# Performance work log

Measured on AMD Instinct MI355X. Metric: run time of the kernel, lower is better.

Reference implementation:

```python
import jax, jax.numpy as jnp
import numpy as np

HIDDEN = 128; HEADS = 8; HD = HIDDEN // HEADS; NRBF = 50; NLAYERS = 6
CUT = 5.0; MAXZ = 100
N = 5000; E = 100000


def cosine_cutoff(d):
    # cutoff_lower = 0: 0.5*(cos(pi*d/cut)+1) * (d < cut)
    return 0.5 * (jnp.cos(d * (jnp.pi / CUT)) + 1.0) * (d < CUT)


def expnorm_rbf(d, means, betas):
    # ExpNormalSmearing with cutoff_lower=0, alpha = 5/cutoff
    alpha = 5.0 / CUT
    return cosine_cutoff(d)[:, None] * jnp.exp(-betas * (jnp.exp(-alpha * d)[:, None] - means) ** 2)


def layernorm(x, w, b):
    m = x.mean(-1, keepdims=True)
    v = ((x - m) ** 2).mean(-1, keepdims=True)
    return (x - m) / jnp.sqrt(v + 1e-5) * w + b


def setup_inputs():
    key = jax.random.key(0)
    ks = jax.random.split(key, 16)
    start = float(np.exp(-CUT))

    def lin(k, fi, fo):
        return jax.random.normal(k, (fi, fo), jnp.float32) / np.sqrt(fi)

    def lin_l(k, fi, fo):
        return jax.random.normal(k, (NLAYERS, fi, fo), jnp.float32) / np.sqrt(fi)

    return {
        "z": jax.random.randint(ks[0], (N,), 0, MAXZ),
        "edge_index": jax.random.randint(ks[1], (2, E), 0, N),
        "edge_vec": jax.random.normal(ks[2], (E, 3), jnp.float32) * 1.7,
        "emb": jax.random.normal(ks[3], (MAXZ, HIDDEN), jnp.float32),
        "means": jnp.linspace(start, 1.0, NRBF, dtype=jnp.float32),
        "betas": jnp.full((NRBF,), (2.0 / NRBF * (1.0 - start)) ** -2, dtype=jnp.float32),
        "ne_emb": jax.random.normal(ks[4], (MAXZ, HIDDEN), jnp.float32),
        "dpW": lin(ks[5], NRBF, HIDDEN), "dpb": jnp.zeros((HIDDEN,), jnp.float32),
        "cbW": lin(ks[6], 2 * HIDDEN, HIDDEN), "cbb": jnp.zeros((HIDDEN,), jnp.float32),
        "lnw": jnp.ones((NLAYERS, HIDDEN), jnp.float32), "lnb": jnp.zeros((NLAYERS, HIDDEN), jnp.float32),
        "qW": lin_l(ks[7], HIDDEN, HIDDEN), "qb": jnp.zeros((NLAYERS, HIDDEN), jnp.float32),
        "kW": lin_l(ks[8], HIDDEN, HIDDEN), "kb": jnp.zeros((NLAYERS, HIDDEN), jnp.float32),
        "vW": lin_l(ks[9], HIDDEN, 3 * HIDDEN), "vb": jnp.zeros((NLAYERS, 3 * HIDDEN), jnp.float32),
        "oW": lin_l(ks[10], HIDDEN, 3 * HIDDEN), "ob": jnp.zeros((NLAYERS, 3 * HIDDEN), jnp.float32),
        "vecW": lin_l(ks[11], HIDDEN, 3 * HIDDEN),
        "dkW": lin_l(ks[12], NRBF, HIDDEN), "dkb": jnp.zeros((NLAYERS, HIDDEN), jnp.float32),
        "dvW": lin_l(ks[13], NRBF, 3 * HIDDEN), "dvb": jnp.zeros((NLAYERS, 3 * HIDDEN), jnp.float32),
        "onw": jnp.ones((HIDDEN,), jnp.float32), "onb": jnp.zeros((HIDDEN,), jnp.float32),
    }


def _forward(z, edge_index, edge_vec, emb, means, betas, ne_emb, dpW, dpb, cbW, cbb,
             lnw, lnb, qW, qb, kW, kb, vW, vb, oW, ob, vecW, dkW, dkb, dvW, dvb, onw, onb):
    src, dst = edge_index[0], edge_index[1]          # j (source), i (target)
    n = z.shape[0]
    x = emb[z]                                        # [N, H]
    ew = jnp.linalg.norm(edge_vec, axis=1)            # [E]
    ea = expnorm_rbf(ew, means, betas)                # [E, NRBF]
    nonself = src != dst
    # normalize edge vectors except self-loop edges (kept as-is, matching the torch clone/mask)
    evn = edge_vec / jnp.where(nonself, ew, 1.0)[:, None]
    cut_e = cosine_cutoff(ew)                         # [E]

    # --- NeighborEmbedding: self-loops removed from aggregation ---
    W = (ea @ dpW + dpb) * cut_e[:, None]
    W = jnp.where(nonself[:, None], W, 0.0)
    agg = jax.ops.segment_sum(ne_emb[z][src] * W, dst, num_segments=n)
    x = jnp.concatenate([x, agg], axis=1) @ cbW + cbb
    vec = jnp.zeros((n, 3, HIDDEN), x.dtype)

    def layer(carry, p):
        x, vec = carry
        h = layernorm(x, p["lnw"], p["lnb"])
        q = (h @ p["qW"] + p["qb"]).reshape(n, HEADS, HD)
        k = (h @ p["kW"] + p["kb"]).reshape(n, HEADS, HD)
        v = (h @ p["vW"] + p["vb"]).reshape(n, HEADS, 3 * HD)
        vec1, vec2, vec3 = jnp.split(jnp.einsum("nch,hk->nck", vec, p["vecW"]), 3, axis=-1)
        vec_dot = (vec1 * vec2).sum(axis=1)                    # [N, H]
        vec_h = vec.reshape(n, 3, HEADS, HD)
        dk = jax.nn.silu(ea @ p["dkW"] + p["dkb"]).reshape(-1, HEADS, HD)
        dv = jax.nn.silu(ea @ p["dvW"] + p["dvb"]).reshape(-1, HEADS, 3 * HD)
        # per-edge attention weight, silu activation, smoothly cut off
        attn = jax.nn.silu((q[dst] * k[src] * dk).sum(-1)) * cut_e[:, None]   # [E, heads]
        xm, w1, w2 = jnp.split(v[src] * dv, 3, axis=2)                        # each [E, heads, HD]
        xm = xm * attn[:, :, None]
        vecm = vec_h[src] * w1[:, None] + w2[:, None] * evn[:, :, None, None] # [E, 3, heads, HD]
        xa = jax.ops.segment_sum(xm, dst, num_segments=n).reshape(n, HIDDEN)
        va = jax.ops.segment_sum(vecm, dst, num_segments=n).reshape(n, 3, HIDDEN)
        o1, o2, o3 = jnp.split(xa @ p["oW"] + p["ob"], 3, axis=-1)
        dx = vec_dot * o2 + o3
        dvec = vec3 * o1[:, None, :] + va
        return (x + dx, vec + dvec), None

    stacked = {"lnw": lnw, "lnb": lnb, "qW": qW, "qb": qb, "kW": kW, "kb": kb,
               "vW": vW, "vb": vb, "oW": oW, "ob": ob, "vecW": vecW,
               "dkW": dkW, "dkb": dkb, "dvW": dvW, "dvb": dvb}
    (x, vec), _ = jax.lax.scan(layer, (x, vec), stacked)
    x = layernorm(x, onw, onb)
    return x, vec


def reference(z, edge_index, edge_vec, emb, means, betas, ne_emb, dpW, dpb, cbW, cbb,
              lnw, lnb, qW, qb, kW, kb, vW, vb, oW, ob, vecW, dkW, dkb, dvW, dvb, onw, onb):
    return _forward(z, edge_index, edge_vec, emb, means, betas, ne_emb, dpW, dpb, cbW, cbb,
                    lnw, lnb, qW, qb, kW, kb, vW, vb, oW, ob, vecW, dkW, dkb, dvW, dvb, onw, onb)
```

## Files before the change

kernel.cpp:

```cpp
#include <hip/hip_runtime.h>
#include <math.h>

#define HID 128
#define NRBF 50
#define NLAYERS 6
#define CUTV 5.0f
#define KNOTS 1024
#define TSCALE 204.8f
#define TINV   0.0048828125f
#define TROWS  (KNOTS + 1)
#define TRWORDS 512
#define TSTRIDE ((size_t)TROWS * TRWORDS)
#define WCOLS 1408
#define KB 16

typedef unsigned int  uint32;
typedef unsigned short ushort16;
typedef __attribute__((ext_vector_type(8))) short short8;
typedef __attribute__((ext_vector_type(4))) float f32x4;

__device__ __forceinline__ float siluf(float x){ return x / (1.0f + __expf(-x)); }
__device__ __forceinline__ float lerpf(float a, float b, float f){ return fmaf(f, b - a, a); }
__device__ __forceinline__ ushort16 f2b(float x){
    uint32 u = __float_as_uint(x);
    u += 0x7fffu + ((u >> 16) & 1u);
    return (ushort16)(u >> 16);
}
__device__ __forceinline__ float b2f(ushort16 u){ return __uint_as_float(((uint32)u) << 16); }
__device__ __forceinline__ uint32 packp(float a, float b){
    return (uint32)f2b(a) | ((uint32)f2b(b) << 16);
}
__device__ __forceinline__ float plo(uint32 u){ return __uint_as_float(u << 16); }
__device__ __forceinline__ float phi(uint32 u){ return __uint_as_float(u & 0xffff0000u); }
__device__ __forceinline__ float plerp(uint32 u, float f){ float a = plo(u); return fmaf(f, phi(u) - a, a); }

__global__ void k_zero(int* p, int n){
    int i = blockIdx.x*blockDim.x + threadIdx.x;
    if (i < n) p[i] = 0;
}

__global__ void k_count(const int* ei, int E, int* counts){
    int e = blockIdx.x*blockDim.x + threadIdx.x;
    if (e < E) atomicAdd(&counts[ei[E + e]], 1);
}

__global__ void k_scan(const int* counts, int* offsets, int* cursor, int n){
    __shared__ int part[1024];
    int tid = threadIdx.x;
    int PER = (n + 1023) >> 10;
    int base = tid * PER;
    int loc[8]; int s = 0;
    #pragma unroll 8
    for (int ii = 0; ii < 8; ii++){
        if (ii < PER){
            int idx = base + ii;
            int c = (idx < n) ? counts[idx] : 0;
            loc[ii] = s; s += c;
        }
    }
    part[tid] = s;
    __syncthreads();
    for (int off = 1; off < 1024; off <<= 1){
        int v = (tid >= off) ? part[tid - off] : 0;
        __syncthreads();
        part[tid] += v;
        __syncthreads();
    }
    int excl = (tid == 0) ? 0 : part[tid - 1];
    #pragma unroll 8
    for (int ii = 0; ii < 8; ii++){
        if (ii < PER){
            int idx = base + ii;
            if (idx < n){ int o = excl + loc[ii]; offsets[idx] = o; cursor[idx] = o; }
        }
    }
    if (tid == 1023) offsets[n] = part[1023];
}

__global__ void k_scatter(const int* ei, int E, int* cursor, int* eperm){
    int e = blockIdx.x*blockDim.x + threadIdx.x;
    if (e < E){
        int d = ei[E + e];
        int pos = atomicAdd(&cursor[d], 1);
        eperm[pos] = e;
    }
}

__global__ __launch_bounds__(256) void k_srcsort(const int* offsets, const int* ei, int* eperm, int N){
    int node = blockIdx.x*4 + (threadIdx.x >> 6);
    int lane = threadIdx.x & 63;
    if (node >= N) return;
    int r0 = offsets[node], r1 = offsets[node+1];
    for (int c0 = r0; c0 < r1; c0 += 64){
        int n = min(64, r1 - c0);
        int e = 0; int key = 0x7fffffff;
        if (lane < n){ e = eperm[c0 + lane]; key = ei[e]; }
        int rank = 0;
        for (int t = 0; t < n; t++){
            int kt = __shfl(key, t, 64);
            if (t != lane && ((kt < key) || (kt == key && t < lane))) rank++;
        }
        if (lane < n) eperm[c0 + rank] = e;
    }
}

__global__ void k_edge_vals(const int* ei, const float* edge_vec, const int* eperm, int E,
                            int4* edata, float4* evn4){
    int row = blockIdx.x*blockDim.x + threadIdx.x;
    if (row >= E) return;
    int e = eperm[row];
    int s = ei[e], d = ei[E + e];
    float vx = edge_vec[e*3+0], vy = edge_vec[e*3+1], vz = edge_vec[e*3+2];
    float ew = sqrtf(vx*vx + vy*vy + vz*vz);
    float cut = (ew < CUTV) ? 0.5f*(__cosf(ew * 0.62831853071795864f) + 1.0f) : 0.0f;
    int ns = (s != d) ? 1 : 0;
    float inv = ns ? (1.0f/ew) : 1.0f;
    float un = fminf(ew * TSCALE, (float)KNOTS);
    int j = (int)un;
    float f = un - (float)j;
    int4 ed; ed.x = s; ed.y = j; ed.z = __float_as_int(f); ed.w = __float_as_int(cut);
    edata[row] = ed;
    float4 ev; ev.x = vx*inv; ev.y = vy*inv; ev.z = vz*inv; ev.w = ns ? 1.0f : 0.0f;
    evn4[row] = ev;
}

__global__ void k_pad(ushort16* hb16, ushort16* vecm, ushort16* xab16, int N, int Nup, int N3up){
    int i = blockIdx.x*blockDim.x + threadIdx.x;
    int hpad = (Nup - N)*HID;
    int vpad = (N3up - 3*N)*HID;
    if (i < hpad){ hb16[(size_t)N*HID + i] = 0; xab16[(size_t)N*HID + i] = 0; }
    if (i < vpad) vecm[(size_t)3*N*HID + i] = 0;
}

__global__ __launch_bounds__(512) void k_build_tables(
    const float* means, const float* betas,
    const float* dkW, const float* dkb, const float* dvW, const float* dvb,
    uint32* Tp){
    int jb = blockIdx.x * KB;
    int l  = blockIdx.y;
    int c  = threadIdx.x;
    __shared__ float ea_s[KB+1][NRBF+2];
    for (int idx = c; idx < (KB+1)*NRBF; idx += 512){
        int kk = idx / NRBF, r = idx - kk*NRBF;
        float d = (jb + kk) * TINV;
        float cut = (d < CUTV) ? 0.5f*(__cosf(d * 0.62831853071795864f) + 1.0f) : 0.0f;
        float u = __expf(-d) - means[r];
        ea_s[kk][r] = cut * __expf(-betas[r]*u*u);
    }
    __syncthreads();
    int h = c >> 2, i = c & 3;
    const float* Wcol; int stride; float bias;
    if (i == 0){
        Wcol = dkW + (size_t)l*NRBF*HID + h; stride = HID;
        bias = dkb[(size_t)l*HID + h];
    } else {
        int col = ((h >> 4)*48 + (h & 15)) + 16*(i-1);
        Wcol = dvW + (size_t)l*NRBF*384 + col; stride = 384;
        bias = dvb[(size_t)l*384 + col];
    }
    float a[KB+1];
    #pragma unroll
    for (int k = 0; k <= KB; k++) a[k] = bias;
    for (int r = 0; r < NRBF; r++){
        float w = Wcol[(size_t)r*stride];
        #pragma unroll
        for (int k = 0; k <= KB; k++) a[k] += ea_s[k][r]*w;
    }
    uint32* dst = Tp + (size_t)l*TSTRIDE + (size_t)jb*TRWORDS + c;
    float sp = siluf(a[0]);
    #pragma unroll
    for (int k = 0; k < KB; k++){
        int j = jb + k;
        if (j >= TROWS) break;
        float sn = siluf(a[k+1]);
        dst[(size_t)k*TRWORDS] = packp(sp, sn);
        sp = sn;
    }
}

__global__ __launch_bounds__(128) void k_build_ne(
    const float* means, const float* betas,
    const float* dpW, const float* dpb, float2* Tne){
    int j = blockIdx.x, c = threadIdx.x;
    __shared__ float ea0[NRBF], ea1[NRBF];
    float d0 = j * TINV, d1 = (j+1) * TINV;
    float c0 = (d0 < CUTV) ? 0.5f*(__cosf(d0 * 0.62831853071795864f) + 1.0f) : 0.0f;
    float c1 = (d1 < CUTV) ? 0.5f*(__cosf(d1 * 0.62831853071795864f) + 1.0f) : 0.0f;
    if (c < NRBF){
        float m = means[c], be = betas[c];
        float u0 = __expf(-d0) - m, u1 = __expf(-d1) - m;
        ea0[c] = c0 * __expf(-be*u0*u0);
        ea1[c] = c1 * __expf(-be*u1*u1);
    }
    __syncthreads();
    float a0 = dpb[c], a1 = a0;
    #pragma unroll
    for (int r = 0; r < NRBF; r++){ float w = dpW[r*HID + c]; a0 += ea0[r]*w; a1 += ea1[r]*w; }
    float2 o; o.x = a0*c0; o.y = a1*c1;
    Tne[(size_t)j*HID + c] = o;
}

__global__ __launch_bounds__(256) void k_build_wt(
    const float* qW, const float* kW, const float* vW, const float* vecW, const float* oW,
    ushort16* WT){
    int l = blockIdx.y; int c0 = blockIdx.x*32;
    __shared__ ushort16 t[128][33];
    for (int i = threadIdx.x; i < 128*32; i += 256){
        int k = i >> 5, c = i & 31;
        int gcol = c0 + c;
        const float* W; int C; int oc;
        if (gcol < 128)      { W = qW   + (size_t)l*HID*128; C = 128; oc = gcol; }
        else if (gcol < 640) {
            int s = gcol - 128; int h = s >> 2, si = s & 3;
            if (si == 3){ W = kW + (size_t)l*HID*128; C = 128; oc = h; }
            else        { W = vW + (size_t)l*HID*384; C = 384; oc = (h>>4)*48 + (h&15) + 16*si; }
        }
        else if (gcol < 1024){ W = vecW + (size_t)l*HID*384; C = 384; oc = gcol-640; }
        else                 { W = oW   + (size_t)l*HID*384; C = 384; oc = gcol-1024; }
        t[k][c] = f2b(W[(size_t)k*C + oc]);
    }
    __syncthreads();
    ushort16* dst = WT + (size_t)l*WCOLS*HID + (size_t)c0*HID;
    for (int i = threadIdx.x; i < 128*32; i += 256){
        int c = i >> 7, k = i & 127;
        dst[(size_t)c*HID + k] = t[k][c];
    }
}

__global__ __launch_bounds__(512) void k_build_bias(
    const float* kb, const float* vb, float* kvbias){
    int l = blockIdx.x, s = threadIdx.x;
    int h = s >> 2, i = s & 3;
    float v = (i == 3) ? kb[(size_t)l*HID + h]
                       : vb[(size_t)l*384 + (h>>4)*48 + (h&15) + 16*i];
    kvbias[(size_t)l*512 + s] = v;
}

__global__ __launch_bounds__(256) void k_mfma01(
    const ushort16* __restrict__ hb16, const ushort16* __restrict__ vecm,
    const ushort16* __restrict__ WT, const float* __restrict__ qbias,
    const float* __restrict__ kvbias,
    float* __restrict__ qo, ushort16* __restrict__ vpack,
    ushort16* __restrict__ vecout, int N){
    int cg = blockIdx.x;
    int rblk = blockIdx.y*64;
    const ushort16* A; int R; int cblk; const ushort16* wt;
    if (cg < 10){ A = hb16; R = N;   cblk = cg*64;      wt = WT; }
    else        { A = vecm; R = 3*N; cblk = (cg-10)*64; wt = WT + (size_t)640*HID; }
    if (rblk >= R) return;
    int wave = threadIdx.x >> 6, lane = threadIdx.x & 63;
    int r0 = rblk + wave*16;
    int l16 = lane & 15, lg = lane >> 4;
    short8 a[4];
    const ushort16* ar = A + (size_t)(r0 + l16)*HID + lg*8;
    #pragma unroll
    for (int ks = 0; ks < 4; ks++) a[ks] = *(const short8*)(ar + ks*32);
    f32x4 acc[4];
    #pragma unroll
    for (int ct = 0; ct < 4; ct++){ acc[ct][0]=0.f; acc[ct][1]=0.f; acc[ct][2]=0.f; acc[ct][3]=0.f; }
    #pragma unroll
    for (int ct = 0; ct < 4; ct++){
        const ushort16* br = wt + (size_t)(cblk + ct*16 + l16)*HID + lg*8;
        #pragma unroll
        for (int ks = 0; ks < 4; ks++){
            short8 b = *(const short8*)(br + ks*32);
            acc[ct] = __builtin_amdgcn_mfma_f32_16x16x32_bf16(a[ks], b, acc[ct], 0, 0, 0);
        }
    }
    __shared__ ushort16 lds[64][72];
    if (cg < 2){
        #pragma unroll
        for (int ct = 0; ct < 4; ct++){
            int gc = cblk + ct*16 + l16;
            float bb = qbias[gc];
            #pragma unroll
            for (int rg = 0; rg < 4; rg++){
                int row = r0 + lg*4 + rg;
                if (row < R) qo[(size_t)row*HID + gc] = acc[ct][rg] + bb;
            }
        }
        return;
    }
    const float* bias = (cg < 10) ? (kvbias + (cblk - 128)) : nullptr;
    #pragma unroll
    for (int ct = 0; ct < 4; ct++){
        int lc = ct*16 + l16;
        float bb = bias ? bias[lc] : 0.f;
        #pragma unroll
        for (int rg = 0; rg < 4; rg++)
            lds[wave*16 + lg*4 + rg][lc] = f2b(acc[ct][rg] + bb);
    }
    __syncthreads();
    ushort16* out; int stride, colbase;
    if (cg < 10){ out = vpack;  stride = 512; colbase = cblk - 128; }
    else        { out = vecout; stride = 384; colbase = cblk; }
    const uint32* l32 = (const uint32*)&lds[0][0];
    #pragma unroll
    for (int it = 0; it < 8; it++){
        int idx = it*256 + threadIdx.x;
        int row = idx >> 5, cp = idx & 31;
        int grow = rblk + row;
        if (grow < R){
            uint32 val = l32[row*36 + cp];
            *((uint32*)(out + (size_t)grow*stride + colbase) + cp) = val;
        }
    }
}

__global__ __launch_bounds__(128) void k_ne_agg(
    const int* offsets, const int4* edata, const float4* evn4, const float2* Tne,
    const int* z, const float* ne_emb, float* agg){
    int i = blockIdx.x, h = threadIdx.x;
    float acc = 0.f;
    int r0 = offsets[i], r1 = offsets[i+1];
    #pragma unroll 4
    for (int row = r0; row < r1; row++){
        int4 ed = edata[row];
        int s = ed.x, j = ed.y;
        float f = __int_as_float(ed.z);
        float mask = evn4[row].w;
        float2 tv = Tne[(size_t)j*HID + h];
        float w = lerpf(tv.x, tv.y, f) * mask;
        acc += w * ne_emb[(size_t)z[s]*HID + h];
    }
    agg[(size_t)i*HID + h] = acc;
}

__global__ __launch_bounds__(128) void k_combine_ln(
    const int* z, const float* emb, const float* agg, const float* cbW, const float* cbb,
    const float* lnw0, const float* lnb0,
    float* x, ushort16* hb16, float* vec, ushort16* vecm, uint32* vecpack, int N){
    int n0 = blockIdx.x*8, h = threadIdx.x;
    __shared__ float in_s[8][2*HID];
    int nr = min(8, N - n0);
    for (int m = 0; m < nr; m++){
        in_s[m][h]       = emb[(size_t)z[n0+m]*HID + h];
        in_s[m][HID + h] = agg[(size_t)(n0+m)*HID + h];
    }
    __syncthreads();
    float acc[8];
    #pragma unroll
    for (int m = 0; m < 8; m++) acc[m] = 0.f;
    for (int kk = 0; kk < 2*HID; kk += 4){
        float w0 = cbW[(kk+0)*HID + h], w1 = cbW[(kk+1)*HID + h];
        float w2 = cbW[(kk+2)*HID + h], w3 = cbW[(kk+3)*HID + h];
        #pragma unroll
        for (int m = 0; m < 8; m++){
            const float* a = &in_s[m][kk];
            acc[m] += a[0]*w0 + a[1]*w1 + a[2]*w2 + a[3]*w3;
        }
    }
    float bias = cbb[h], w = lnw0[h], bb = lnb0[h];
    __shared__ float r1_[2], r2_[2];
    int wid = h >> 6;
    for (int m = 0; m < nr; m++){
        int n = n0 + m;
        float v = acc[m] + bias;
        x[(size_t)n*HID + h] = v;
        float s1 = v, s2 = v*v;
        #pragma unroll
        for (int o = 32; o; o >>= 1){ s1 += __shfl_xor(s1, o, 64); s2 += __shfl_xor(s2, o, 64); }
        if ((h & 63) == 0){ r1_[wid] = s1; r2_[wid] = s2; }
        __syncthreads();
        float sum = r1_[0] + r1_[1], sumsq = r2_[0] + r2_[1];
        float mean = sum * (1.f/HID);
        float var = sumsq * (1.f/HID) - mean*mean;
        float inv = rsqrtf(var + 1e-5f);
        hb16[(size_t)n*HID + h] = f2b((v - mean)*inv*w + bb);
        __syncthreads();
        vec [(size_t)n*384 + h]       = 0.f;
        vec [(size_t)n*384 + 128 + h] = 0.f;
        vec [(size_t)n*384 + 256 + h] = 0.f;
        vecm[(size_t)n*384 + h]       = 0;
        vecm[(size_t)n*384 + 128 + h] = 0;
        vecm[(size_t)n*384 + 256 + h] = 0;
        vecpack[(size_t)n*256 + 2*h]     = 0;
        vecpack[(size_t)n*256 + 2*h + 1] = 0;
    }
}

__global__ __launch_bounds__(128) void k_edge_agg(
    const int* __restrict__ offsets, const int4* __restrict__ edata,
    const float4* __restrict__ evn4, const uint32* __restrict__ Tp,
    const float* __restrict__ q, const ushort16* __restrict__ vpack,
    const uint32* __restrict__ vecpack,
    ushort16* __restrict__ xa16, float* __restrict__ va){
    int i = blockIdx.x, h = threadIdx.x;
    float qv = q[(size_t)i*HID + h];
    float axa = 0.f, av0 = 0.f, av1 = 0.f, av2 = 0.f;
    int r0 = offsets[i], r1 = offsets[i+1];
    for (int t0 = r0; t0 < r1; t0 += 4){
        float f_[4], cut_[4], ex_[4], ey_[4], ez_[4];
        uint4 t4_[4];
        uint2 vp_[4], vc_[4];
        #pragma unroll
        for (int u = 0; u < 4; u++){
            int row = min(t0 + u, r1 - 1);
            int4 ed = edata[row];
            int s = ed.x, j = ed.y;
            f_[u]   = __int_as_float(ed.z);
            cut_[u] = __int_as_float(ed.w);
            t4_[u] = *(const uint4*)(Tp + (size_t)j*TRWORDS + 4*h);
            vp_[u] = *(const uint2*)(vpack + (size_t)s*512 + 4*h);
            vc_[u] = *(const uint2*)(vecpack + (size_t)s*256 + 2*h);
            float4 ev = evn4[row];
            ex_[u] = ev.x; ey_[u] = ev.y; ez_[u] = ev.z;
        }
        #pragma unroll
        for (int u = 0; u < 4; u++){
            if (t0 + u >= r1) break;
            float f = f_[u];
            float dk = plerp(t4_[u].x, f);
            float kv = phi(vp_[u].y);
            float p = qv * kv * dk;
            p += __shfl_xor(p, 1, 64);
            p += __shfl_xor(p, 2, 64);
            p += __shfl_xor(p, 4, 64);
            p += __shfl_xor(p, 8, 64);
            float attn = siluf(p) * cut_[u];
            float dv0 = plerp(t4_[u].y, f);
            float dv1 = plerp(t4_[u].z, f);
            float dv2 = plerp(t4_[u].w, f);
            axa += plo(vp_[u].x) * dv0 * attn;
            float w1v = phi(vp_[u].x) * dv1;
            float w2v = plo(vp_[u].y) * dv2;
            av0 += plo(vc_[u].x)*w1v + w2v*ex_[u];
            av1 += phi(vc_[u].x)*w1v + w2v*ey_[u];
            av2 += plo(vc_[u].y)*w1v + w2v*ez_[u];
        }
    }
    xa16[(size_t)i*HID + h] = f2b(axa);
    va[(size_t)i*384 + h]       = av0;
    va[(size_t)i*384 + 128 + h] = av1;
    va[(size_t)i*384 + 256 + h] = av2;
}

#define OROWS 32
__global__ __launch_bounds__(256) void k_oupd(
    const ushort16* __restrict__ xab16, const ushort16* __restrict__ WT,
    const float* __restrict__ obias,
    float* __restrict__ x, float* __restrict__ vec, ushort16* __restrict__ vecm,
    uint32* __restrict__ vecpack,
    const ushort16* __restrict__ vecout, const float* __restrict__ va,
    const float* __restrict__ lnw_n, const float* __restrict__ lnb_n,
    ushort16* __restrict__ hb16, float* __restrict__ outx, float* __restrict__ outv,
    int N, int fin){
    __shared__ float o_s[OROWS][385];
    int tile = blockIdx.x; int r0 = tile*OROWS;
    int wid = threadIdx.x >> 6, lane = threadIdx.x & 63;
    int l16 = lane & 15, lg = lane >> 4;
    {
        int rr = r0 + (wid & 1)*16;
        const ushort16* ar = xab16 + (size_t)(rr + l16)*HID + lg*8;
        short8 a[4];
        #pragma unroll
        for (int ks = 0; ks < 4; ks++) a[ks] = *(const short8*)(ar + ks*32);
        int cbase = (wid >> 1)*192;
        const ushort16* wt = WT + (size_t)1024*HID;
        #pragma unroll
        for (int ct = 0; ct < 12; ct++){
            f32x4 acc; acc[0]=0.f; acc[1]=0.f; acc[2]=0.f; acc[3]=0.f;
            const ushort16* br = wt + (size_t)(cbase + ct*16 + l16)*HID + lg*8;
            #pragma unroll
            for (int ks = 0; ks < 4; ks++){
                short8 b = *(const short8*)(br + ks*32);
                acc = __builtin_amdgcn_mfma_f32_16x16x32_bf16(a[ks], b, acc, 0, 0, 0);
            }
            int gc = cbase + ct*16 + l16;
            float bb = obias[gc];
            #pragma unroll
            for (int rg = 0; rg < 4; rg++)
                o_s[(wid & 1)*16 + lg*4 + rg][gc] = acc[rg] + bb;
        }
    }
    __syncthreads();
    for (int pass = 0; pass < 8; pass++){
        int nrow = pass*4 + wid;
        int n = r0 + nrow;
        if (n >= N) break;
        const ushort16* vo = vecout + (size_t)n*1152;
        const float* o_r = o_s[nrow];
        size_t vb = (size_t)n*384;
        float xva, xvb, v0a, v0b, v1a, v1b, v2a, v2b;
        #pragma unroll
        for (int half = 0; half < 2; half++){
            int hh = lane + half*64;
            float vdot = b2f(vo[hh])*b2f(vo[128+hh]) + b2f(vo[384+hh])*b2f(vo[512+hh])
                       + b2f(vo[768+hh])*b2f(vo[896+hh]);
            float o1 = o_r[hh], o2 = o_r[128+hh], o3 = o_r[256+hh];
            float xv = x[(size_t)n*HID + hh] + vdot*o2 + o3;
            float v0 = vec[vb + hh]       + b2f(vo[256  + hh])*o1 + va[vb + hh];
            float v1 = vec[vb + 128 + hh] + b2f(vo[640  + hh])*o1 + va[vb + 128 + hh];
            float v2 = vec[vb + 256 + hh] + b2f(vo[1024 + hh])*o1 + va[vb + 256 + hh];
            if (half == 0){ xva = xv; v0a = v0; v1a = v1; v2a = v2; }
            else          { xvb = xv; v0b = v0; v1b = v1; v2b = v2; }
        }
        float s1 = xva + xvb, s2 = xva*xva + xvb*xvb;
        #pragma unroll
        for (int o = 32; o; o >>= 1){ s1 += __shfl_xor(s1, o, 64); s2 += __shfl_xor(s2, o, 64); }
        float mean = s1 * (1.f/HID);
        float var = s2 * (1.f/HID) - mean*mean;
        float inv = rsqrtf(var + 1e-5f);
        #pragma unroll
        for (int half = 0; half < 2; half++){
            int hh = lane + half*64;
            float xv = half ? xvb : xva;
            float v0 = half ? v0b : v0a;
            float v1 = half ? v1b : v1a;
            float v2 = half ? v2b : v2a;
            float lnv = (xv - mean)*inv*lnw_n[hh] + lnb_n[hh];
            if (!fin){
                x[(size_t)n*HID + hh] = xv;
                vec[vb + hh] = v0; vec[vb + 128 + hh] = v1; vec[vb + 256 + hh] = v2;
                vecm[vb + hh] = f2b(v0); vecm[vb + 128 + hh] = f2b(v1); vecm[vb + 256 + hh] = f2b(v2);
                vecpack[(size_t)n*256 + 2*hh]     = packp(v0, v1);
                vecpack[(size_t)n*256 + 2*hh + 1] = packp(v2, 0.f);
                hb16[(size_t)n*HID + hh] = f2b(lnv);
            } else {
                outx[(size_t)n*HID + hh] = lnv;
                outv[vb + hh] = v0; outv[vb + 128 + hh] = v1; outv[vb + 256 + hh] = v2;
            }
        }
    }
}

extern "C" void kernel_launch(void* const* d_in, const int* in_sizes, int n_in,
                              void* d_out, int out_size, void* d_ws, size_t ws_size,
                              hipStream_t stream){
    const int*   z        = (const int*)  d_in[0];
    const int*   ei       = (const int*)  d_in[1];
    const float* edge_vec = (const float*)d_in[2];
    const float* emb      = (const float*)d_in[3];
    const float* means    = (const float*)d_in[4];
    const float* betas    = (const float*)d_in[5];
    const float* ne_emb   = (const float*)d_in[6];
    const float* dpW      = (const float*)d_in[7];
    const float* dpb      = (const float*)d_in[8];
    const float* cbW      = (const float*)d_in[9];
    const float* cbb      = (const float*)d_in[10];
    const float* lnw      = (const float*)d_in[11];
    const float* lnb      = (const float*)d_in[12];
    const float* qW       = (const float*)d_in[13];
    const float* qb       = (const float*)d_in[14];
    const float* kW       = (const float*)d_in[15];
    const float* kb       = (const float*)d_in[16];
    const float* vW       = (const float*)d_in[17];
    const float* vb       = (const float*)d_in[18];
    const float* oW       = (const float*)d_in[19];
    const float* obias    = (const float*)d_in[20];
    const float* vecW     = (const float*)d_in[21];
    const float* dkW      = (const float*)d_in[22];
    const float* dkb      = (const float*)d_in[23];
    const float* dvW      = (const float*)d_in[24];
    const float* dvb      = (const float*)d_in[25];
    const float* onw      = (const float*)d_in[26];
    const float* onb      = (const float*)d_in[27];

    int N = in_sizes[0];
    int E = in_sizes[1] / 2;
    int Nup  = ((N + 63) >> 6) << 6;
    int N3up = ((3*N + 63) >> 6) << 6;

    char* p = (char*)d_ws;
    auto alloc = [&](size_t bytes){ void* r = (void*)p; p += (bytes + 255) & ~(size_t)255; return r; };
    int*      counts  = (int*)     alloc((size_t)N*4);
    int*      offsets = (int*)     alloc((size_t)(N+1)*4);
    int*      cursor  = (int*)     alloc((size_t)N*4);
    int*      eperm   = (int*)     alloc((size_t)E*4);
    int4*     edata   = (int4*)    alloc((size_t)E*16);
    float4*   evn4    = (float4*)  alloc((size_t)E*16);
    uint32*   Tp      = (uint32*)  alloc((size_t)NLAYERS*TSTRIDE*4);
    float2*   Tne     = (float2*)  alloc((size_t)TROWS*HID*8);
    ushort16* WT      = (ushort16*)alloc((size_t)NLAYERS*WCOLS*HID*2);
    float*    kvbias  = (float*)   alloc((size_t)NLAYERS*512*4);
    float*    agg     = (float*)   alloc((size_t)N*HID*4);
    float*    xb      = (float*)   alloc((size_t)N*HID*4);
    ushort16* hb16    = (ushort16*)alloc((size_t)Nup*HID*2);
    float*    qb_     = (float*)   alloc((size_t)N*HID*4);
    ushort16* vpack   = (ushort16*)alloc((size_t)N*512*2);
    uint32*   vecpack = (uint32*)  alloc((size_t)N*256*4);
    ushort16* vecm    = (ushort16*)alloc((size_t)N3up*HID*2);
    float*    vecb    = (float*)   alloc((size_t)N*384*4);
    ushort16* vecout  = (ushort16*)alloc((size_t)N*1152*2);
    ushort16* xab16   = (ushort16*)alloc((size_t)Nup*HID*2);
    float*    vab     = (float*)   alloc((size_t)N*384*4);

    k_zero<<<(N+255)/256, 256, 0, stream>>>(counts, N);
    k_count<<<(E+255)/256, 256, 0, stream>>>(ei, E, counts);
    k_scan<<<1, 1024, 0, stream>>>(counts, offsets, cursor, N);
    k_scatter<<<(E+255)/256, 256, 0, stream>>>(ei, E, cursor, eperm);
    k_srcsort<<<(N+3)/4, 256, 0, stream>>>(offsets, ei, eperm, N);
    k_edge_vals<<<(E+255)/256, 256, 0, stream>>>(ei, edge_vec, eperm, E, edata, evn4);
    k_pad<<<((Nup-N)*HID + (N3up-3*N)*HID + 255)/256 + 1, 256, 0, stream>>>(hb16, vecm, xab16, N, Nup, N3up);

    k_build_tables<<<dim3((TROWS + KB - 1)/KB, NLAYERS), 512, 0, stream>>>(means, betas, dkW, dkb, dvW, dvb, Tp);
    k_build_ne<<<TROWS, 128, 0, stream>>>(means, betas, dpW, dpb, Tne);
    k_build_wt<<<dim3(WCOLS/32, NLAYERS), 256, 0, stream>>>(qW, kW, vW, vecW, oW, WT);
    k_build_bias<<<NLAYERS, 512, 0, stream>>>(kb, vb, kvbias);
    k_ne_agg<<<N, 128, 0, stream>>>(offsets, edata, evn4, Tne, z, ne_emb, agg);
    k_combine_ln<<<(N+7)/8, 128, 0, stream>>>(z, emb, agg, cbW, cbb, lnw, lnb,
                                              xb, hb16, vecb, vecm, vecpack, N);

    float* outx = (float*)d_out;
    float* outv = (float*)d_out + (size_t)N*HID;

    for (int l = 0; l < NLAYERS; l++){
        const ushort16* WTl = WT + (size_t)l*WCOLS*HID;
        k_mfma01<<<dim3(16, (3*N+63)/64), 256, 0, stream>>>(hb16, vecm, WTl,
            qb + (size_t)l*HID, kvbias + (size_t)l*512,
            qb_, vpack, vecout, N);
        k_edge_agg<<<N, 128, 0, stream>>>(offsets, edata, evn4, Tp + (size_t)l*TSTRIDE,
                                          qb_, vpack, vecpack, xab16, vab);
        int fin = (l == NLAYERS-1);
        k_oupd<<<(N + OROWS - 1)/OROWS, 256, 0, stream>>>(xab16, WTl, obias + (size_t)l*384,
            xb, vecb, vecm, vecpack, vecout, vab,
            fin ? onw : lnw + (size_t)(l+1)*HID,
            fin ? onb : lnb + (size_t)(l+1)*HID,
            hb16, outx, outv, N, fin);
    }
}
```

Baseline: 670.4 us.

## Remap edge-agg to one wavefront per node with two channels per lane

Each node's edge aggregation now runs on a single 64-lane wavefront, packed four nodes per 256-thread block, and each lane handles channels g and g+64. The per-layer tables, q, vpack and vecpack are re-laid out so each lane's two channels sit next to each other, which allows wider 128-bit loads. This halves the number of edge-metadata loads and loop iterations per channel and cuts the block count. The producing kernels must write the new interleaved layout consistently, and the extra registers may lower occupancy.

After: 704.7 us. 5.1% more time.

```diff
diff --git a/kernel.cpp b/kernel.cpp
--- a/kernel.cpp
+++ b/kernel.cpp
@@ -166,7 +166,8 @@
         #pragma unroll
         for (int k = 0; k <= KB; k++) a[k] += ea_s[k][r]*w;
     }
-    uint32* dst = Tp + (size_t)l*TSTRIDE + (size_t)jb*TRWORDS + c;
+    int slot = (h & 63)*8 + (h >> 6)*4 + i;
+    uint32* dst = Tp + (size_t)l*TSTRIDE + (size_t)jb*TRWORDS + slot;
     float sp = siluf(a[0]);
     #pragma unroll
     for (int k = 0; k < KB; k++){
@@ -273,10 +274,11 @@
         for (int ct = 0; ct < 4; ct++){
             int gc = cblk + ct*16 + l16;
             float bb = qbias[gc];
+            int qslot = (gc & 63)*2 + (gc >> 6);
             #pragma unroll
             for (int rg = 0; rg < 4; rg++){
                 int row = r0 + lg*4 + rg;
-                if (row < R) qo[(size_t)row*HID + gc] = acc[ct][rg] + bb;
+                if (row < R) qo[(size_t)row*HID + qslot] = acc[ct][rg] + bb;
             }
         }
         return;
@@ -291,18 +293,32 @@
             lds[wave*16 + lg*4 + rg][lc] = f2b(acc[ct][rg] + bb);
     }
     __syncthreads();
-    ushort16* out; int stride, colbase;
-    if (cg < 10){ out = vpack;  stride = 512; colbase = cblk - 128; }
-    else        { out = vecout; stride = 384; colbase = cblk; }
     const uint32* l32 = (const uint32*)&lds[0][0];
-    #pragma unroll
-    for (int it = 0; it < 8; it++){
-        int idx = it*256 + threadIdx.x;
-        int row = idx >> 5, cp = idx & 31;
-        int grow = rblk + row;
-        if (grow < R){
-            uint32 val = l32[row*36 + cp];
-            *((uint32*)(out + (size_t)grow*stride + colbase) + cp) = val;
+    if (cg < 10){
+        int colbase = cblk - 128;
+        #pragma unroll
+        for (int it = 0; it < 8; it++){
+            int idx = it*256 + threadIdx.x;
+            int row = idx >> 5, cp = idx & 31;
+            int grow = rblk + row;
+            if (grow < R){
+                uint32 val = l32[row*36 + cp];
+                int s0 = colbase + 2*cp;
+                int hh = s0 >> 2, w = (s0 & 3) >> 1;
+                int slot = (hh & 63)*4 + (hh >> 6)*2 + w;
+                ((uint32*)(vpack + (size_t)grow*512))[slot] = val;
+            }
+        }
+    } else {
+        #pragma unroll
+        for (int it = 0; it < 8; it++){
+            int idx = it*256 + threadIdx.x;
+            int row = idx >> 5, cp = idx & 31;
+            int grow = rblk + row;
+            if (grow < R){
+                uint32 val = l32[row*36 + cp];
+                *((uint32*)(vecout + (size_t)grow*384 + cblk) + cp) = val;
+            }
         }
     }
 }
@@ -379,20 +395,22 @@
     }
 }
 
-__global__ __launch_bounds__(128) void k_edge_agg(
+__global__ __launch_bounds__(256) void k_edge_agg(
     const int* __restrict__ offsets, const int4* __restrict__ edata,
     const float4* __restrict__ evn4, const uint32* __restrict__ Tp,
     const float* __restrict__ q, const ushort16* __restrict__ vpack,
     const uint32* __restrict__ vecpack,
-    ushort16* __restrict__ xa16, float* __restrict__ va){
-    int i = blockIdx.x, h = threadIdx.x;
-    float qv = q[(size_t)i*HID + h];
-    float axa = 0.f, av0 = 0.f, av1 = 0.f, av2 = 0.f;
-    int r0 = offsets[i], r1 = offsets[i+1];
+    ushort16* __restrict__ xa16, float* __restrict__ va, int N){
+    int node = blockIdx.x*4 + (threadIdx.x >> 6);
+    int g = threadIdx.x & 63;
+    if (node >= N) return;
+    float2 qv = *(const float2*)(q + (size_t)node*HID + 2*g);
+    float axaA = 0.f, av0A = 0.f, av1A = 0.f, av2A = 0.f;
+    float axaB = 0.f, av0B = 0.f, av1B = 0.f, av2B = 0.f;
+    int r0 = offsets[node], r1 = offsets[node+1];
     for (int t0 = r0; t0 < r1; t0 += 4){
         float f_[4], cut_[4], ex_[4], ey_[4], ez_[4];
-        uint4 t4_[4];
-        uint2 vp_[4], vc_[4];
+        uint4 ta_[4], tb_[4], vp_[4], vc_[4];
         #pragma unroll
         for (int u = 0; u < 4; u++){
             int row = min(t0 + u, r1 - 1);
@@ -400,39 +418,49 @@
             int s = ed.x, j = ed.y;
             f_[u]   = __int_as_float(ed.z);
             cut_[u] = __int_as_float(ed.w);
-            t4_[u] = *(const uint4*)(Tp + (size_t)j*TRWORDS + 4*h);
-            vp_[u] = *(const uint2*)(vpack + (size_t)s*512 + 4*h);
-            vc_[u] = *(const uint2*)(vecpack + (size_t)s*256 + 2*h);
+            const uint32* tp = Tp + (size_t)j*TRWORDS + 8*g;
+            ta_[u] = *(const uint4*)(tp);
+            tb_[u] = *(const uint4*)(tp + 4);
+            vp_[u] = *(const uint4*)((const uint32*)(vpack + (size_t)s*512) + 4*g);
+            vc_[u] = *(const uint4*)(vecpack + (size_t)s*256 + 4*g);
             float4 ev = evn4[row];
             ex_[u] = ev.x; ey_[u] = ev.y; ez_[u] = ev.z;
         }
         #pragma unroll
         for (int u = 0; u < 4; u++){
             if (t0 + u >= r1) break;
-            float f = f_[u];
-            float dk = plerp(t4_[u].x, f);
-            float kv = phi(vp_[u].y);
-            float p = qv * kv * dk;
-            p += __shfl_xor(p, 1, 64);
-            p += __shfl_xor(p, 2, 64);
-            p += __shfl_xor(p, 4, 64);
-            p += __shfl_xor(p, 8, 64);
-            float attn = siluf(p) * cut_[u];
-            float dv0 = plerp(t4_[u].y, f);
-            float dv1 = plerp(t4_[u].z, f);
-            float dv2 = plerp(t4_[u].w, f);
-            axa += plo(vp_[u].x) * dv0 * attn;
-            float w1v = phi(vp_[u].x) * dv1;
-            float w2v = plo(vp_[u].y) * dv2;
-            av0 += plo(vc_[u].x)*w1v + w2v*ex_[u];
-            av1 += phi(vc_[u].x)*w1v + w2v*ey_[u];
-            av2 += plo(vc_[u].y)*w1v + w2v*ez_[u];
-        }
-    }
-    xa16[(size_t)i*HID + h] = f2b(axa);
-    va[(size_t)i*384 + h]       = av0;
-    va[(size_t)i*384 + 128 + h] = av1;
-    va[(size_t)i*384 + 256 + h] = av2;
+            float f = f_[u], cut = cut_[u];
+            float kA = phi(vp_[u].y);
+            float pA = qv.x * kA * plerp(ta_[u].x, f);
+            float kB = phi(vp_[u].w);
+            float pB = qv.y * kB * plerp(tb_[u].x, f);
+            pA += __shfl_xor(pA, 1, 64); pB += __shfl_xor(pB, 1, 64);
+            pA += __shfl_xor(pA, 2, 64); pB += __shfl_xor(pB, 2, 64);
+            pA += __shfl_xor(pA, 4, 64); pB += __shfl_xor(pB, 4, 64);
+            pA += __shfl_xor(pA, 8, 64); pB += __shfl_xor(pB, 8, 64);
+            float attnA = siluf(pA) * cut;
+            float attnB = siluf(pB) * cut;
+            axaA += plo(vp_[u].x) * plerp(ta_[u].y, f) * attnA;
+            axaB += plo(vp_[u].z) * plerp(tb_[u].y, f) * attnB;
+            float w1A = phi(vp_[u].x) * plerp(ta_[u].z, f);
+            float w2A = plo(vp_[u].y) * plerp(ta_[u].w, f);
+            float w1B = phi(vp_[u].z) * plerp(tb_[u].z, f);
+            float w2B = plo(vp_[u].w) * plerp(tb_[u].w, f);
+            float ex = ex_[u], ey = ey_[u], ez = ez_[u];
+            av0A += plo(vc_[u].x)*w1A + w2A*ex;
+            av1A += phi(vc_[u].x)*w1A + w2A*ey;
+            av2A += plo(vc_[u].y)*w1A + w2A*ez;
+            av0B += plo(vc_[u].z)*w1B + w2B*ex;
+            av1B += phi(vc_[u].z)*w1B + w2B*ey;
+            av2B += plo(vc_[u].w)*w1B + w2B*ez;
+        }
+    }
+    xa16[(size_t)node*HID + g]      = f2b(axaA);
+    xa16[(size_t)node*HID + g + 64] = f2b(axaB);
+    float* var_ = va + (size_t)node*384;
+    var_[g]            = av0A; var_[g + 64]       = av0B;
+    var_[128 + g]      = av1A; var_[128 + g + 64] = av1B;
+    var_[256 + g]      = av2A; var_[256 + g + 64] = av2B;
 }
 
 #define OROWS 32
@@ -513,8 +541,9 @@
                 x[(size_t)n*HID + hh] = xv;
                 vec[vb + hh] = v0; vec[vb + 128 + hh] = v1; vec[vb + 256 + hh] = v2;
                 vecm[vb + hh] = f2b(v0); vecm[vb + 128 + hh] = f2b(v1); vecm[vb + 256 + hh] = f2b(v2);
-                vecpack[(size_t)n*256 + 2*hh]     = packp(v0, v1);
-                vecpack[(size_t)n*256 + 2*hh + 1] = packp(v2, 0.f);
+                int gg = hh & 63, hf = hh >> 6;
+                vecpack[(size_t)n*256 + gg*4 + hf*2]     = packp(v0, v1);
+                vecpack[(size_t)n*256 + gg*4 + hf*2 + 1] = packp(v2, 0.f);
                 hb16[(size_t)n*HID + hh] = f2b(lnv);
             } else {
                 outx[(size_t)n*HID + hh] = lnv;
@@ -609,8 +638,8 @@
         k_mfma01<<<dim3(16, (3*N+63)/64), 256, 0, stream>>>(hb16, vecm, WTl,
             qb + (size_t)l*HID, kvbias + (size_t)l*512,
             qb_, vpack, vecout, N);
-        k_edge_agg<<<N, 128, 0, stream>>>(offsets, edata, evn4, Tp + (size_t)l*TSTRIDE,
-                                          qb_, vpack, vecpack, xab16, vab);
+        k_edge_agg<<<(N+3)/4, 256, 0, stream>>>(offsets, edata, evn4, Tp + (size_t)l*TSTRIDE,
+                                                qb_, vpack, vecpack, xab16, vab, N);
         int fin = (l == NLAYERS-1);
         k_oupd<<<(N + OROWS - 1)/OROWS, 256, 0, stream>>>(xab16, WTl, obias + (size_t)l*384,
             xb, vecb, vecm, vecpack, vecout, vab,
```

## Compact mfma01 grid, bf16-pack neighbor-embedding tables, batch ne_agg loads

Applied to the files above, without the earlier changes.

The k_mfma01 launch becomes a flat 1D grid with no early-exit blocks, so the many empty blocks the 2D grid spent on the hidden-state columns go away. The neighbor-embedding table and the per-node gathered ne_emb are stored as packed bf16, which halves the gather traffic in k_ne_agg. That loop now issues four edges' loads before accumulating, and masks self-loops by comparing the source index instead of reading evn4. The zero kernel is replaced with hipMemsetAsync; bf16 storage adds some rounding in the initial embedding.

Measured after the change: 615.2 us. 8.2% less time.

```diff
diff --git a/kernel.cpp b/kernel.cpp
--- a/kernel.cpp
+++ b/kernel.cpp
@@ -33,11 +33,6 @@
 __device__ __forceinline__ float plo(uint32 u){ return __uint_as_float(u << 16); }
 __device__ __forceinline__ float phi(uint32 u){ return __uint_as_float(u & 0xffff0000u); }
 __device__ __forceinline__ float plerp(uint32 u, float f){ float a = plo(u); return fmaf(f, phi(u) - a, a); }
-
-__global__ void k_zero(int* p, int n){
-    int i = blockIdx.x*blockDim.x + threadIdx.x;
-    if (i < n) p[i] = 0;
-}
 
 __global__ void k_count(const int* ei, int E, int* counts){
     int e = blockIdx.x*blockDim.x + threadIdx.x;
@@ -132,6 +127,13 @@
     if (i < vpad) vecm[(size_t)3*N*HID + i] = 0;
 }
 
+__global__ void k_prep_nemb(const int* z, const float* ne_emb, ushort16* nemb16, int total){
+    int idx = blockIdx.x*256 + threadIdx.x;
+    if (idx >= total) return;
+    int n = idx >> 7, h = idx & 127;
+    nemb16[idx] = f2b(ne_emb[(size_t)z[n]*HID + h]);
+}
+
 __global__ __launch_bounds__(512) void k_build_tables(
     const float* means, const float* betas,
     const float* dkW, const float* dkb, const float* dvW, const float* dvb,
@@ -180,7 +182,7 @@
 
 __global__ __launch_bounds__(128) void k_build_ne(
     const float* means, const float* betas,
-    const float* dpW, const float* dpb, float2* Tne){
+    const float* dpW, const float* dpb, uint32* Tne32){
     int j = blockIdx.x, c = threadIdx.x;
     __shared__ float ea0[NRBF], ea1[NRBF];
     float d0 = j * TINV, d1 = (j+1) * TINV;
@@ -196,8 +198,7 @@
     float a0 = dpb[c], a1 = a0;
     #pragma unroll
     for (int r = 0; r < NRBF; r++){ float w = dpW[r*HID + c]; a0 += ea0[r]*w; a1 += ea1[r]*w; }
-    float2 o; o.x = a0*c0; o.y = a1*c1;
-    Tne[(size_t)j*HID + c] = o;
+    Tne32[(size_t)j*HID + c] = packp(a0*c0, a1*c1);
 }
 
 __global__ __launch_bounds__(256) void k_build_wt(
@@ -242,12 +243,15 @@
     const float* __restrict__ kvbias,
     float* __restrict__ qo, ushort16* __restrict__ vpack,
     ushort16* __restrict__ vecout, int N){
-    int cg = blockIdx.x;
-    int rblk = blockIdx.y*64;
+    int NT1 = (N + 63) >> 6;
+    int NT3 = (3*N + 63) >> 6;
+    int b = blockIdx.x;
+    int cg, rblk;
+    if (b < 10*NT1){ cg = b / NT1; rblk = (b - cg*NT1)*64; }
+    else { int b2 = b - 10*NT1; int c2 = b2 / NT3; cg = 10 + c2; rblk = (b2 - c2*NT3)*64; }
     const ushort16* A; int R; int cblk; const ushort16* wt;
     if (cg < 10){ A = hb16; R = N;   cblk = cg*64;      wt = WT; }
     else        { A = vecm; R = 3*N; cblk = (cg-10)*64; wt = WT + (size_t)640*HID; }
-    if (rblk >= R) return;
     int wave = threadIdx.x >> 6, lane = threadIdx.x & 63;
     int r0 = rblk + wave*16;
     int l16 = lane & 15, lg = lane >> 4;
@@ -263,8 +267,8 @@
         const ushort16* br = wt + (size_t)(cblk + ct*16 + l16)*HID + lg*8;
         #pragma unroll
         for (int ks = 0; ks < 4; ks++){
-            short8 b = *(const short8*)(br + ks*32);
-            acc[ct] = __builtin_amdgcn_mfma_f32_16x16x32_bf16(a[ks], b, acc[ct], 0, 0, 0);
+            short8 bfr = *(const short8*)(br + ks*32);
+            acc[ct] = __builtin_amdgcn_mfma_f32_16x16x32_bf16(a[ks], bfr, acc[ct], 0, 0, 0);
         }
     }
     __shared__ ushort16 lds[64][72];
@@ -308,20 +312,28 @@
 }
 
 __global__ __launch_bounds__(128) void k_ne_agg(
-    const int* offsets, const int4* edata, const float4* evn4, const float2* Tne,
-    const int* z, const float* ne_emb, float* agg){
+    const int* __restrict__ offsets, const int4* __restrict__ edata,
+    const uint32* __restrict__ Tne32, const ushort16* __restrict__ nemb16,
+    float* __restrict__ agg){
     int i = blockIdx.x, h = threadIdx.x;
     float acc = 0.f;
     int r0 = offsets[i], r1 = offsets[i+1];
-    #pragma unroll 4
-    for (int row = r0; row < r1; row++){
-        int4 ed = edata[row];
-        int s = ed.x, j = ed.y;
-        float f = __int_as_float(ed.z);
-        float mask = evn4[row].w;
-        float2 tv = Tne[(size_t)j*HID + h];
-        float w = lerpf(tv.x, tv.y, f) * mask;
-        acc += w * ne_emb[(size_t)z[s]*HID + h];
+    for (int t0 = r0; t0 < r1; t0 += 4){
+        uint32 tn_[4]; ushort16 nb_[4]; float f_[4]; int s_[4];
+        #pragma unroll
+        for (int u = 0; u < 4; u++){
+            int row = min(t0 + u, r1 - 1);
+            int4 ed = edata[row];
+            s_[u] = ed.x;
+            f_[u] = __int_as_float(ed.z);
+            tn_[u] = Tne32[(size_t)ed.y*HID + h];
+            nb_[u] = nemb16[(size_t)ed.x*HID + h];
+        }
+        #pragma unroll
+        for (int u = 0; u < 4; u++){
+            if (t0 + u >= r1) break;
+            if (s_[u] != i) acc += plerp(tn_[u], f_[u]) * b2f(nb_[u]);
+        }
     }
     agg[(size_t)i*HID + h] = acc;
 }
@@ -401,7 +413,7 @@
             f_[u]   = __int_as_float(ed.z);
             cut_[u] = __int_as_float(ed.w);
             t4_[u] = *(const uint4*)(Tp + (size_t)j*TRWORDS + 4*h);
-            vp_[u] = *(const uint2*)(vpack + (size_t)s*512 + 4*h);
+            vp_[u] = *(const uint2*)((const uint32*)(vpack + (size_t)s*512) + 2*h);
             vc_[u] = *(const uint2*)(vecpack + (size_t)s*256 + 2*h);
             float4 ev = evn4[row];
             ex_[u] = ev.x; ey_[u] = ev.y; ez_[u] = ev.z;
@@ -570,9 +582,10 @@
     int4*     edata   = (int4*)    alloc((size_t)E*16);
     float4*   evn4    = (float4*)  alloc((size_t)E*16);
     uint32*   Tp      = (uint32*)  alloc((size_t)NLAYERS*TSTRIDE*4);
-    float2*   Tne     = (float2*)  alloc((size_t)TROWS*HID*8);
+    uint32*   Tne32   = (uint32*)  alloc((size_t)TROWS*HID*4);
     ushort16* WT      = (ushort16*)alloc((size_t)NLAYERS*WCOLS*HID*2);
     float*    kvbias  = (float*)   alloc((size_t)NLAYERS*512*4);
+    ushort16* nemb16  = (ushort16*)alloc((size_t)N*HID*2);
     float*    agg     = (float*)   alloc((size_t)N*HID*4);
     float*    xb      = (float*)   alloc((size_t)N*HID*4);
     ushort16* hb16    = (ushort16*)alloc((size_t)Nup*HID*2);
@@ -585,28 +598,31 @@
     ushort16* xab16   = (ushort16*)alloc((size_t)Nup*HID*2);
     float*    vab     = (float*)   alloc((size_t)N*384*4);
 
-    k_zero<<<(N+255)/256, 256, 0, stream>>>(counts, N);
+    hipMemsetAsync(counts, 0, (size_t)N*4, stream);
     k_count<<<(E+255)/256, 256, 0, stream>>>(ei, E, counts);
     k_scan<<<1, 1024, 0, stream>>>(counts, offsets, cursor, N);
     k_scatter<<<(E+255)/256, 256, 0, stream>>>(ei, E, cursor, eperm);
     k_srcsort<<<(N+3)/4, 256, 0, stream>>>(offsets, ei, eperm, N);
     k_edge_vals<<<(E+255)/256, 256, 0, stream>>>(ei, edge_vec, eperm, E, edata, evn4);
     k_pad<<<((Nup-N)*HID + (N3up-3*N)*HID + 255)/256 + 1, 256, 0, stream>>>(hb16, vecm, xab16, N, Nup, N3up);
+    k_prep_nemb<<<(N*HID+255)/256, 256, 0, stream>>>(z, ne_emb, nemb16, N*HID);
 
     k_build_tables<<<dim3((TROWS + KB - 1)/KB, NLAYERS), 512, 0, stream>>>(means, betas, dkW, dkb, dvW, dvb, Tp);
-    k_build_ne<<<TROWS, 128, 0, stream>>>(means, betas, dpW, dpb, Tne);
+    k_build_ne<<<TROWS, 128, 0, stream>>>(means, betas, dpW, dpb, Tne32);
     k_build_wt<<<dim3(WCOLS/32, NLAYERS), 256, 0, stream>>>(qW, kW, vW, vecW, oW, WT);
     k_build_bias<<<NLAYERS, 512, 0, stream>>>(kb, vb, kvbias);
-    k_ne_agg<<<N, 128, 0, stream>>>(offsets, edata, evn4, Tne, z, ne_emb, agg);
+    k_ne_agg<<<N, 128, 0, stream>>>(offsets, edata, Tne32, nemb16, agg);
     k_combine_ln<<<(N+7)/8, 128, 0, stream>>>(z, emb, agg, cbW, cbb, lnw, lnb,
                                               xb, hb16, vecb, vecm, vecpack, N);
 
     float* outx = (float*)d_out;
     float* outv = (float*)d_out + (size_t)N*HID;
 
+    int NT1 = (N + 63) >> 6;
+    int NT3 = (3*N + 63) >> 6;
     for (int l = 0; l < NLAYERS; l++){
         const ushort16* WTl = WT + (size_t)l*WCOLS*HID;
-        k_mfma01<<<dim3(16, (3*N+63)/64), 256, 0, stream>>>(hb16, vecm, WTl,
+        k_mfma01<<<10*NT1 + 6*NT3, 256, 0, stream>>>(hb16, vecm, WTl,
             qb + (size_t)l*HID, kvbias + (size_t)l*512,
             qb_, vpack, vecout, N);
         k_edge_agg<<<N, 128, 0, stream>>>(offsets, edata, evn4, Tp + (size_t)l*TSTRIDE,
```
